# Performance work log

Measured on AMD Instinct MI355X. Metric: run time of the kernel, lower is better.

Reference implementation:

```python
import jax, jax.numpy as jnp
import numpy as np

N_NODES = 50000
N_EDGES = 800000
N_REL = 3
N_GRAPHS = 500
EMB = 128
IN_DIM = EMB * 3
HID = 256
N_CLASS = 10
N_SHAPE, N_COLOR, MAX_POS = 8, 8, 128


def rgcn_layer(h, src, dst, etype, W, root, b):
    """PyG RGCNConv with default aggr='mean':
    out[v] = sum_r mean_{(j->v) in E_r} h[j] @ W[r] + h[v] @ root + b
    Aggregate raw features per (dst, relation) bucket, then apply relation matmuls.
    """
    N, R = h.shape[0], W.shape[0]
    seg = dst * R + etype  # combined (node, relation) segment id
    sums = jax.ops.segment_sum(h[src], seg, num_segments=N * R)          # (N*R, d)
    cnt = jax.ops.segment_sum(jnp.ones(seg.shape, h.dtype), seg, num_segments=N * R)
    mean = (sums / jnp.maximum(cnt, 1.0)[:, None]).reshape(N, R, -1)     # (N, R, d)
    return jnp.einsum('nrd,rdh->nh', mean, W) + h @ root + b


def setup_inputs() -> dict:
    key = jax.random.key(0)
    ks = jax.random.split(key, 20)
    f32 = jnp.float32
    inp = {
        's': jax.random.randint(ks[0], (N_NODES,), 0, N_SHAPE),
        'c': jax.random.randint(ks[1], (N_NODES,), 0, N_COLOR),
        'p': jax.random.randint(ks[2], (N_NODES,), 0, MAX_POS),
        'edge_index': jax.random.randint(ks[3], (2, N_EDGES), 0, N_NODES),
        'edge_type': jax.random.randint(ks[4], (N_EDGES,), 0, N_REL),
        'batch': jnp.sort(jax.random.randint(ks[5], (N_NODES,), 0, N_GRAPHS)),
        'shape_emb': jax.random.normal(ks[6], (N_SHAPE, EMB), f32),
        'color_emb': jax.random.normal(ks[7], (N_COLOR, EMB), f32),
        'pos_emb': jax.random.normal(ks[8], (MAX_POS, EMB), f32),
        'W1': jax.random.normal(ks[9], (N_REL, IN_DIM, HID), f32) / np.sqrt(IN_DIM),
        'root1': jax.random.normal(ks[10], (IN_DIM, HID), f32) / np.sqrt(IN_DIM),
        'b1': jnp.zeros((HID,), f32),
        'W2': jax.random.normal(ks[11], (N_REL, HID, HID), f32) / np.sqrt(HID),
        'root2': jax.random.normal(ks[12], (HID, HID), f32) / np.sqrt(HID),
        'b2': jnp.zeros((HID,), f32),
        'lin_w': jax.random.normal(ks[13], (HID, N_CLASS), f32) / np.sqrt(HID),
        'lin_b': jnp.zeros((N_CLASS,), f32),
    }
    return inp


def reference(s, c, p, edge_index, edge_type, batch,
              shape_emb, color_emb, pos_emb,
              W1, root1, b1, W2, root2, b2, lin_w, lin_b):
    src, dst = edge_index[0], edge_index[1]
    h = jnp.concatenate([shape_emb[s], color_emb[c], pos_emb[p]], axis=-1)  # (N, 3*emb)
    h = jax.nn.relu(rgcn_layer(h, src, dst, edge_type, W1, root1, b1))
    h = jax.nn.relu(rgcn_layer(h, src, dst, edge_type, W2, root2, b2))
    # global_mean_pool over graphs
    gsum = jax.ops.segment_sum(h, batch, num_segments=N_GRAPHS)
    gcnt = jax.ops.segment_sum(jnp.ones((h.shape[0],), h.dtype), batch, num_segments=N_GRAPHS)
    pooled = gsum / jnp.maximum(gcnt, 1.0)[:, None]
    return pooled @ lin_w + lin_b
```

## Files before the change

kernel.cpp:

```cpp
#include <hip/hip_runtime.h>
#include <hip/hip_bf16.h>

#define NN 50000
#define NE 800000
#define NR 3
#define NG 500
#define NB (NN * NR)
#define NCLS 10
#define NCMB 8192
#define CHUNK 2048
#define NBLK ((NB + CHUNK - 1) / CHUNK)

#define P1_COMBO   196
#define P1_ZCNT    586
#define P1_ZPOOL   502
#define P1_TAB     576
#define P1_WF      1024
#define P1_TOTAL   (P1_COMBO + P1_ZCNT + P1_ZPOOL + P1_TAB + P1_WF)
#define P2_CNT     3125
#define P2_COMB    (4 * NCMB)
#define P2_TOTAL   (P2_CNT + P2_COMB)

typedef __hip_bfloat16 bf16;
typedef __attribute__((ext_vector_type(8))) short short8;
typedef __attribute__((ext_vector_type(4))) float floatx4;

static __device__ __forceinline__ float b2f(bf16 x) { return __bfloat162float(x); }
static __device__ __forceinline__ bf16  f2b(float x) { return __float2bfloat16(x); }
static __device__ __forceinline__ float bs2f(short x) {
    return __bfloat162float(*reinterpret_cast<const bf16*>(&x));
}
static __device__ __forceinline__ short f2bs(float x) {
    bf16 b = __float2bfloat16(x);
    return *reinterpret_cast<const short*>(&b);
}

__global__ __launch_bounds__(256) void prep1(const int* __restrict__ s,
                                             const int* __restrict__ c,
                                             const int* __restrict__ p,
                                             const float* __restrict__ se,
                                             const float* __restrict__ ce,
                                             const float* __restrict__ pe,
                                             const float* __restrict__ W1,
                                             const float* __restrict__ root1,
                                             const float* __restrict__ W2,
                                             const float* __restrict__ root2,
                                             int* __restrict__ combo,
                                             unsigned* __restrict__ cnt,
                                             unsigned* __restrict__ poolz,
                                             float* __restrict__ tab,
                                             bf16* __restrict__ Wf) {
    int b = blockIdx.x, t = threadIdx.x;
    if (b < P1_COMBO) {
        int n = b * 256 + t;
        if (n < NN) combo[n] = (s[n] << 10) | (c[n] << 7) | p[n];
        return;
    }
    b -= P1_COMBO;
    if (b < P1_ZCNT) {
        int i = b * 256 + t;
        if (i < NB) cnt[i] = 0u;
        return;
    }
    b -= P1_ZCNT;
    if (b < P1_ZPOOL) {
        int i = b * 256 + t;
        if (i < NG * 256 + NG) poolz[i] = 0u;
        return;
    }
    b -= P1_ZPOOL;
    if (b < P1_TAB) {
        int r = b / 144, row = b % 144;
        const float* A; int segk;
        if (row < 8)       { A = se + row * 128;        segk = 0; }
        else if (row < 16) { A = ce + (row - 8) * 128;  segk = 128; }
        else               { A = pe + (row - 16) * 128; segk = 256; }
        const float* W = (r < 3) ? (W1 + (size_t)r * 384 * 256) : root1;
        float acc = 0.f;
        for (int k = 0; k < 128; ++k)
            acc += A[k] * W[(size_t)(segk + k) * 256 + t];
        tab[((size_t)r * 144 + row) * 256 + t] = acc;
        return;
    }
    b -= P1_TAB;
    {
        int idx = b * 256 + t;
        int j     = idx & 7;
        int lane  = (idx >> 3) & 63;
        int ni    = (idx >> 9) & 3;
        int chunk = (idx >> 11) & 31;
        int colblk = idx >> 16;
        int col = colblk * 64 + ni * 16 + (lane & 15);
        int k   = chunk * 32 + (lane >> 4) * 8 + j;
        float v = (k < 768) ? W2[((size_t)(k >> 8) * 256 + (k & 255)) * 256 + col]
                            : root2[(size_t)(k - 768) * 256 + col];
        Wf[idx] = f2b(v);
    }
}

__global__ __launch_bounds__(256) void prep2(const int* __restrict__ ei,
                                             const int* __restrict__ et,
                                             int* __restrict__ cnt,
                                             const float* __restrict__ tab,
                                             const float* __restrict__ b1,
                                             bf16* __restrict__ comb) {
    int b = blockIdx.x, t = threadIdx.x;
    if (b < P2_CNT) {
        int e = b * 256 + t;
        if (e < NE) atomicAdd(&cnt[ei[NE + e] * NR + et[e]], 1);
        return;
    }
    b -= P2_CNT;
    {
        int r = b >> 13, cmb = b & (NCMB - 1);
        int si = cmb >> 10, ci = (cmb >> 7) & 7, pi = cmb & 127;
        const float* tr = tab + (size_t)r * 144 * 256;
        float v = tr[si * 256 + t] + tr[(8 + ci) * 256 + t] + tr[(16 + pi) * 256 + t];
        if (r == 3) v += b1[t];
        comb[(size_t)b * 256 + t] = f2b(v);
    }
}

__global__ __launch_bounds__(256) void scan_block_sums(const int* __restrict__ cnt,
                                                       int* __restrict__ bsum) {
    __shared__ int sm[256];
    int b = blockIdx.x, t = threadIdx.x;
    int base = b * CHUNK + t * 8, s = 0;
#pragma unroll
    for (int j = 0; j < 8; ++j) { int i = base + j; if (i < NB) s += cnt[i]; }
    sm[t] = s; __syncthreads();
    for (int st = 128; st; st >>= 1) { if (t < st) sm[t] += sm[t + st]; __syncthreads(); }
    if (!t) bsum[b] = sm[0];
}

__global__ __launch_bounds__(256) void scan_write(const int* __restrict__ cnt,
                                                  const int* __restrict__ bsum,
                                                  int* __restrict__ off,
                                                  int* __restrict__ cursor) {
    int b = blockIdx.x, t = threadIdx.x;
    int bbase = 0;
    for (int i = 0; i < b; ++i) bbase += bsum[i];
    if (b == 0 && t == 0) {
        int tot = 0;
        for (int i = 0; i < NBLK; ++i) tot += bsum[i];
        off[NB] = tot;
    }
    int base = b * CHUNK + t * 8;
    int v[8], ts = 0;
#pragma unroll
    for (int j = 0; j < 8; ++j) { int i = base + j; v[j] = (i < NB) ? cnt[i] : 0; ts += v[j]; }
    int lane = t & 63, wv = t >> 6;
    int incl = ts;
    for (int d = 1; d < 64; d <<= 1) {
        int o = __shfl_up(incl, d, 64);
        if (lane >= d) incl += o;
    }
    __shared__ int wsum[4];
    if (lane == 63) wsum[wv] = incl;
    __syncthreads();
    int wbase = 0;
    for (int w = 0; w < wv; ++w) wbase += wsum[w];
    int run = bbase + wbase + incl - ts;
#pragma unroll
    for (int j = 0; j < 8; ++j) {
        int i = base + j;
        if (i < NB) { off[i] = run; cursor[i] = run; }
        run += v[j];
    }
}

__global__ __launch_bounds__(256) void scatter_edges(const int* __restrict__ ei,
                                                     const int* __restrict__ et,
                                                     const int* __restrict__ combo,
                                                     int* __restrict__ cursor,
                                                     int2* __restrict__ esc) {
    int e = blockIdx.x * 256 + threadIdx.x;
    if (e >= NE) return;
    int b = ei[NE + e] * NR + et[e];
    int pos = atomicAdd(&cursor[b], 1);
    int s = ei[e];
    esc[pos] = make_int2(s, combo[s]);
}

__global__ __launch_bounds__(256) void l1_fused(const int* __restrict__ off,
                                                const int2* __restrict__ esc,
                                                const int* __restrict__ combo,
                                                const bf16* __restrict__ comb,
                                                bf16* __restrict__ h1) {
    int wave = threadIdx.x >> 6, lane = threadIdx.x & 63;
    int dst = blockIdx.x * 4 + wave;
    if (dst >= NN) return;
    int half = lane >> 5, li8 = (lane & 31) * 8;
    int o0 = off[dst * NR],     o1 = off[dst * NR + 1],
        o2 = off[dst * NR + 2], o3 = off[dst * NR + 3];
    short8 rootv = {};
    if (half == 0)
        rootv = *(const short8*)(comb + ((size_t)(3 * NCMB) + combo[dst]) * 256 + li8);
    const bf16* c0 = comb;
    const bf16* c1 = comb + (size_t)NCMB * 256;
    const bf16* c2 = comb + (size_t)2 * NCMB * 256;
    float s0[8] = {}, s1[8] = {}, s2[8] = {};
    int n = max((o1 - o0 + 1) >> 1, max((o2 - o1 + 1) >> 1, (o3 - o2 + 1) >> 1));
    for (int k = 0; k < n; k += 2) {
#pragma unroll
        for (int kk = 0; kk < 2; ++kk) {
            int i0 = o0 + 2 * (k + kk) + half;
            int i1 = o1 + 2 * (k + kk) + half;
            int i2 = o2 + 2 * (k + kk) + half;
            bool g0 = i0 < o1, g1 = i1 < o2, g2 = i2 < o3;
            int2 e0 = esc[g0 ? i0 : 0];
            int2 e1 = esc[g1 ? i1 : 0];
            int2 e2 = esc[g2 ? i2 : 0];
            short8 v0 = *(const short8*)(c0 + (size_t)(g0 ? e0.y : 0) * 256 + li8);
            short8 v1 = *(const short8*)(c1 + (size_t)(g1 ? e1.y : 0) * 256 + li8);
            short8 v2 = *(const short8*)(c2 + (size_t)(g2 ? e2.y : 0) * 256 + li8);
            float m0 = g0 ? 1.f : 0.f, m1 = g1 ? 1.f : 0.f, m2 = g2 ? 1.f : 0.f;
#pragma unroll
            for (int i = 0; i < 8; ++i) {
                s0[i] += bs2f(v0[i]) * m0;
                s1[i] += bs2f(v1[i]) * m1;
                s2[i] += bs2f(v2[i]) * m2;
            }
        }
    }
    float inv0 = (o1 > o0) ? 1.f / (float)(o1 - o0) : 0.f;
    float inv1 = (o2 > o1) ? 1.f / (float)(o2 - o1) : 0.f;
    float inv2 = (o3 > o2) ? 1.f / (float)(o3 - o2) : 0.f;
    short8 o;
#pragma unroll
    for (int i = 0; i < 8; ++i) {
        float t0 = s0[i] + __shfl_xor(s0[i], 32);
        float t1 = s1[i] + __shfl_xor(s1[i], 32);
        float t2 = s2[i] + __shfl_xor(s2[i], 32);
        float a = bs2f(rootv[i]) + t0 * inv0 + t1 * inv1 + t2 * inv2;
        o[i] = f2bs(fmaxf(a, 0.f));
    }
    if (half == 0)
        *(short8*)(h1 + (size_t)dst * 256 + li8) = o;
}

__global__ __launch_bounds__(256) void agg_all(const int* __restrict__ off,
                                               const int2* __restrict__ esc,
                                               const bf16* __restrict__ h1,
                                               bf16* __restrict__ hagg) {
    int wave = threadIdx.x >> 6, lane = threadIdx.x & 63;
    int dst = blockIdx.x * 4 + wave;
    if (dst >= NN) return;
    int half = lane >> 5, li8 = (lane & 31) * 8;
    int o0 = off[dst * NR],     o1 = off[dst * NR + 1],
        o2 = off[dst * NR + 2], o3 = off[dst * NR + 3];
    float s0[8] = {}, s1[8] = {}, s2[8] = {};
    int n = max((o1 - o0 + 1) >> 1, max((o2 - o1 + 1) >> 1, (o3 - o2 + 1) >> 1));
    for (int k = 0; k < n; k += 2) {
#pragma unroll
        for (int kk = 0; kk < 2; ++kk) {
            int i0 = o0 + 2 * (k + kk) + half;
            int i1 = o1 + 2 * (k + kk) + half;
            int i2 = o2 + 2 * (k + kk) + half;
            bool g0 = i0 < o1, g1 = i1 < o2, g2 = i2 < o3;
            int2 e0 = esc[g0 ? i0 : 0];
            int2 e1 = esc[g1 ? i1 : 0];
            int2 e2 = esc[g2 ? i2 : 0];
            short8 v0 = *(const short8*)(h1 + (size_t)(g0 ? e0.x : 0) * 256 + li8);
            short8 v1 = *(const short8*)(h1 + (size_t)(g1 ? e1.x : 0) * 256 + li8);
            short8 v2 = *(const short8*)(h1 + (size_t)(g2 ? e2.x : 0) * 256 + li8);
            float m0 = g0 ? 1.f : 0.f, m1 = g1 ? 1.f : 0.f, m2 = g2 ? 1.f : 0.f;
#pragma unroll
            for (int i = 0; i < 8; ++i) {
                s0[i] += bs2f(v0[i]) * m0;
                s1[i] += bs2f(v1[i]) * m1;
                s2[i] += bs2f(v2[i]) * m2;
            }
        }
    }
    float inv0 = (o1 > o0) ? 1.f / (float)(o1 - o0) : 0.f;
    float inv1 = (o2 > o1) ? 1.f / (float)(o2 - o1) : 0.f;
    float inv2 = (o3 > o2) ? 1.f / (float)(o3 - o2) : 0.f;
    short8 w0, w1, w2;
#pragma unroll
    for (int i = 0; i < 8; ++i) {
        float t0 = s0[i] + __shfl_xor(s0[i], 32);
        float t1 = s1[i] + __shfl_xor(s1[i], 32);
        float t2 = s2[i] + __shfl_xor(s2[i], 32);
        w0[i] = f2bs(t0 * inv0);
        w1[i] = f2bs(t1 * inv1);
        w2[i] = f2bs(t2 * inv2);
    }
    if (half == 0) {
        bf16* hd = hagg + (size_t)dst * 768 + li8;
        *(short8*)(hd)       = w0;
        *(short8*)(hd + 256) = w1;
        *(short8*)(hd + 512) = w2;
    }
}

__global__ __launch_bounds__(256) void gemm_cat(const bf16* __restrict__ hagg,
                                                const bf16* __restrict__ h1,
                                                const bf16* __restrict__ Wf,
                                                const float* __restrict__ bias,
                                                const int* __restrict__ batch,
                                                float* __restrict__ pool,
                                                float* __restrict__ gcnt) {
    __shared__ short lds[4][2][32 * 40];
    const int t = threadIdx.x;
    const int wave = t >> 6, lane = t & 63;
    const int quad = lane >> 4, l16 = lane & 15;
    const int row0 = blockIdx.x * 32;
    const int colblk = wave;
    const int rsub = lane >> 2;
    const int ksub = (lane & 3) * 8;
    short* A0 = lds[wave][0];
    short* A1 = lds[wave][1];

    const int r0 = min(row0 + rsub, NN - 1);
    const int r1 = min(row0 + 16 + rsub, NN - 1);
    const bf16* gA0 = hagg + (size_t)r0 * 768 + ksub;
    const bf16* gA1 = hagg + (size_t)r1 * 768 + ksub;
    const bf16* gH0 = h1 + (size_t)r0 * 256 + ksub;
    const bf16* gH1 = h1 + (size_t)r1 * 256 + ksub;
    const short8* bbase = (const short8*)Wf + (size_t)colblk * 32 * 4 * 64 + lane;

    auto loadA2 = [&](int k0, short8& a0, short8& a1) {
        if (k0 < 768) { a0 = *(const short8*)(gA0 + k0); a1 = *(const short8*)(gA1 + k0); }
        else          { a0 = *(const short8*)(gH0 + k0 - 768); a1 = *(const short8*)(gH1 + k0 - 768); }
    };
    auto loadB = [&](int chunk, short8* bf4) {
        const short8* bp = bbase + (size_t)chunk * 4 * 64;
#pragma unroll
        for (int ni = 0; ni < 4; ++ni) bf4[ni] = bp[ni * 64];
    };

    floatx4 acc[2][4] = {};
    short8 aE0, aE1, bE[4];
    short8 aO0, aO1, bO[4];
    loadA2(0, aE0, aE1);  loadB(0, bE);
    loadA2(32, aO0, aO1); loadB(1, bO);

#pragma unroll
    for (int i = 0; i < 32; i += 2) {
        *(short8*)&A0[rsub * 40 + ksub] = aE0;
        *(short8*)&A0[(16 + rsub) * 40 + ksub] = aE1;
        {
            short8 af0 = *(const short8*)&A0[l16 * 40 + quad * 8];
            short8 af1 = *(const short8*)&A0[(16 + l16) * 40 + quad * 8];
#pragma unroll
            for (int ni = 0; ni < 4; ++ni) {
                acc[0][ni] = __builtin_amdgcn_mfma_f32_16x16x32_bf16(af0, bE[ni], acc[0][ni], 0, 0, 0);
                acc[1][ni] = __builtin_amdgcn_mfma_f32_16x16x32_bf16(af1, bE[ni], acc[1][ni], 0, 0, 0);
            }
        }
        if (i + 2 < 32) { loadA2((i + 2) * 32, aE0, aE1); loadB(i + 2, bE); }
        *(short8*)&A1[rsub * 40 + ksub] = aO0;
        *(short8*)&A1[(16 + rsub) * 40 + ksub] = aO1;
        {
            short8 af0 = *(const short8*)&A1[l16 * 40 + quad * 8];
            short8 af1 = *(const short8*)&A1[(16 + l16) * 40 + quad * 8];
#pragma unroll
            for (int ni = 0; ni < 4; ++ni) {
                acc[0][ni] = __builtin_amdgcn_mfma_f32_16x16x32_bf16(af0, bO[ni], acc[0][ni], 0, 0, 0);
                acc[1][ni] = __builtin_amdgcn_mfma_f32_16x16x32_bf16(af1, bO[ni], acc[1][ni], 0, 0, 0);
            }
        }
        if (i + 3 < 32) { loadA2((i + 3) * 32, aO0, aO1); loadB(i + 3, bO); }
    }

    __syncthreads();
    short* st = &lds[0][0][0];
#pragma unroll
    for (int mi = 0; mi < 2; ++mi) {
#pragma unroll
        for (int ni = 0; ni < 4; ++ni) {
            int n = colblk * 64 + ni * 16 + l16;
            float bn = bias[n];
#pragma unroll
            for (int ii = 0; ii < 4; ++ii) {
                int lrow = mi * 16 + quad * 4 + ii;
                float v = (row0 + lrow < NN) ? fmaxf(acc[mi][ni][ii] + bn, 0.f) : 0.f;
                st[lrow * 260 + n] = f2bs(v);
            }
        }
    }
    __syncthreads();
    int nrows = NN - row0; if (nrows > 32) nrows = 32;
    int curg = batch[row0];
    float a = 0.f, cntf = 0.f;
    for (int rr = 0; rr < nrows; ++rr) {
        int g = batch[row0 + rr];
        if (g != curg) {
            atomicAdd(&pool[(size_t)curg * 256 + t], a);
            if (t == 0) atomicAdd(&gcnt[curg], cntf);
            a = 0.f; cntf = 0.f; curg = g;
        }
        a += bs2f(st[rr * 260 + t]);
        cntf += 1.f;
    }
    atomicAdd(&pool[(size_t)curg * 256 + t], a);
    if (t == 0) atomicAdd(&gcnt[curg], cntf);
}

__global__ __launch_bounds__(256) void final_head(const float* __restrict__ pool,
                                                  const float* __restrict__ gcnt,
                                                  const float* __restrict__ lin_w,
                                                  const float* __restrict__ lin_b,
                                                  float* __restrict__ out) {
    __shared__ float sm[256];
    int g = blockIdx.x, t = threadIdx.x;
    float inv = 1.0f / fmaxf(gcnt[g], 1.0f);
    sm[t] = pool[(size_t)g * 256 + t] * inv;
    __syncthreads();
    if (t < NCLS) {
        float s = lin_b[t];
        for (int d = 0; d < 256; ++d) s += sm[d] * lin_w[d * NCLS + t];
        out[g * NCLS + t] = s;
    }
}

extern "C" void kernel_launch(void* const* d_in, const int* in_sizes, int n_in,
                              void* d_out, int out_size, void* d_ws, size_t ws_size,
                              hipStream_t stream) {
    const int*   s_idx = (const int*)d_in[0];
    const int*   c_idx = (const int*)d_in[1];
    const int*   p_idx = (const int*)d_in[2];
    const int*   ei    = (const int*)d_in[3];
    const int*   et    = (const int*)d_in[4];
    const int*   batch = (const int*)d_in[5];
    const float* se    = (const float*)d_in[6];
    const float* ce    = (const float*)d_in[7];
    const float* pe    = (const float*)d_in[8];
    const float* W1    = (const float*)d_in[9];
    const float* root1 = (const float*)d_in[10];
    const float* b1    = (const float*)d_in[11];
    const float* W2    = (const float*)d_in[12];
    const float* root2 = (const float*)d_in[13];
    const float* b2    = (const float*)d_in[14];
    const float* lin_w = (const float*)d_in[15];
    const float* lin_b = (const float*)d_in[16];
    float* out = (float*)d_out;

    char* w = (char*)d_ws;
    size_t o = 0;
    auto alloc = [&](size_t bytes) -> void* {
        o = (o + 15) & ~(size_t)15;
        void* ptr = w + o;
        o += bytes;
        return ptr;
    };
    bf16*  hagg   = (bf16*) alloc((size_t)NN * 768 * 2);
    bf16*  h1     = (bf16*) alloc((size_t)NN * 256 * 2);
    bf16*  comb   = (bf16*) alloc((size_t)4 * NCMB * 256 * 2);
    int*   combo  = (int*)  alloc((size_t)NN * 4);
    int2*  esc    = (int2*) alloc((size_t)NE * 8);
    int*   cnt    = (int*)  alloc((size_t)NB * 4);
    int*   off    = (int*)  alloc((size_t)(NB + 1) * 4);
    int*   cursor = (int*)  alloc((size_t)NB * 4);
    int*   bsum   = (int*)  alloc((size_t)NBLK * 4);
    float* tab    = (float*)alloc((size_t)4 * 144 * 256 * 4);
    bf16*  Wf     = (bf16*) alloc((size_t)256 * 1024 * 2);
    float* pool   = (float*)alloc((size_t)NG * 256 * 4);
    float* gcnt  = (float*)alloc((size_t)NG * 4);
    (void)ws_size;

    prep1<<<P1_TOTAL, 256, 0, stream>>>(s_idx, c_idx, p_idx, se, ce, pe,
                                        W1, root1, W2, root2,
                                        combo, (unsigned*)cnt, (unsigned*)pool, tab, Wf);
    prep2<<<P2_TOTAL, 256, 0, stream>>>(ei, et, cnt, tab, b1, comb);
    scan_block_sums<<<NBLK, 256, 0, stream>>>(cnt, bsum);
    scan_write<<<NBLK, 256, 0, stream>>>(cnt, bsum, off, cursor);
    scatter_edges<<<(NE + 255) / 256, 256, 0, stream>>>(ei, et, combo, cursor, esc);
    l1_fused<<<(NN + 3) / 4, 256, 0, stream>>>(off, esc, combo, comb, h1);
    agg_all<<<(NN + 3) / 4, 256, 0, stream>>>(off, esc, h1, hagg);
    gemm_cat<<<(NN + 31) / 32, 256, 0, stream>>>(hagg, h1, Wf, b2, batch, pool, gcnt);
    final_head<<<NG, 256, 0, stream>>>(pool, gcnt, lin_w, lin_b, out);
}
```

Before: 383.3 us.

## Pack edge records into 32-bit words and flatten layer-1 gather loop

Edge records shrink from an int2 (source, combo) to one 32-bit word holding the source shifted by 13 bits with the 13-bit combo in the low bits. This halves the edge-array footprint written by the scatter and read by both aggregation kernels. Layer-1 aggregation now walks the node's contiguous edge range for all three relations together, unrolled four ways. Each edge picks its relation table and 1/count weight from its position against the bucket offsets, so lanes no longer idle while they wait for the longest relation. The packing assumes node ids fit in 19 bits and combo ids in 13, which holds for these sizes.

```diff
diff --git a/kernel.cpp b/kernel.cpp
--- a/kernel.cpp
+++ b/kernel.cpp
@@ -173,17 +173,17 @@
                                                      const int* __restrict__ et,
                                                      const int* __restrict__ combo,
                                                      int* __restrict__ cursor,
-                                                     int2* __restrict__ esc) {
+                                                     unsigned* __restrict__ esc) {
     int e = blockIdx.x * 256 + threadIdx.x;
     if (e >= NE) return;
     int b = ei[NE + e] * NR + et[e];
     int pos = atomicAdd(&cursor[b], 1);
     int s = ei[e];
-    esc[pos] = make_int2(s, combo[s]);
+    esc[pos] = ((unsigned)s << 13) | (unsigned)combo[s];
 }
 
 __global__ __launch_bounds__(256) void l1_fused(const int* __restrict__ off,
-                                                const int2* __restrict__ esc,
+                                                const unsigned* __restrict__ esc,
                                                 const int* __restrict__ combo,
                                                 const bf16* __restrict__ comb,
                                                 bf16* __restrict__ h1) {
@@ -191,56 +191,66 @@
     int dst = blockIdx.x * 4 + wave;
     if (dst >= NN) return;
     int half = lane >> 5, li8 = (lane & 31) * 8;
-    int o0 = off[dst * NR],     o1 = off[dst * NR + 1],
-        o2 = off[dst * NR + 2], o3 = off[dst * NR + 3];
+    int b0 = dst * NR;
+    int o0 = off[b0], o1 = off[b0 + 1], o2 = off[b0 + 2], o3 = off[b0 + 3];
+    float inv0 = (o1 > o0) ? 1.f / (float)(o1 - o0) : 0.f;
+    float inv1 = (o2 > o1) ? 1.f / (float)(o2 - o1) : 0.f;
+    float inv2 = (o3 > o2) ? 1.f / (float)(o3 - o2) : 0.f;
     short8 rootv = {};
     if (half == 0)
         rootv = *(const short8*)(comb + ((size_t)(3 * NCMB) + combo[dst]) * 256 + li8);
-    const bf16* c0 = comb;
-    const bf16* c1 = comb + (size_t)NCMB * 256;
-    const bf16* c2 = comb + (size_t)2 * NCMB * 256;
-    float s0[8] = {}, s1[8] = {}, s2[8] = {};
-    int n = max((o1 - o0 + 1) >> 1, max((o2 - o1 + 1) >> 1, (o3 - o2 + 1) >> 1));
-    for (int k = 0; k < n; k += 2) {
-#pragma unroll
-        for (int kk = 0; kk < 2; ++kk) {
-            int i0 = o0 + 2 * (k + kk) + half;
-            int i1 = o1 + 2 * (k + kk) + half;
-            int i2 = o2 + 2 * (k + kk) + half;
-            bool g0 = i0 < o1, g1 = i1 < o2, g2 = i2 < o3;
-            int2 e0 = esc[g0 ? i0 : 0];
-            int2 e1 = esc[g1 ? i1 : 0];
-            int2 e2 = esc[g2 ? i2 : 0];
-            short8 v0 = *(const short8*)(c0 + (size_t)(g0 ? e0.y : 0) * 256 + li8);
-            short8 v1 = *(const short8*)(c1 + (size_t)(g1 ? e1.y : 0) * 256 + li8);
-            short8 v2 = *(const short8*)(c2 + (size_t)(g2 ? e2.y : 0) * 256 + li8);
-            float m0 = g0 ? 1.f : 0.f, m1 = g1 ? 1.f : 0.f, m2 = g2 ? 1.f : 0.f;
-#pragma unroll
-            for (int i = 0; i < 8; ++i) {
-                s0[i] += bs2f(v0[i]) * m0;
-                s1[i] += bs2f(v1[i]) * m1;
-                s2[i] += bs2f(v2[i]) * m2;
-            }
-        }
-    }
-    float inv0 = (o1 > o0) ? 1.f / (float)(o1 - o0) : 0.f;
-    float inv1 = (o2 > o1) ? 1.f / (float)(o2 - o1) : 0.f;
-    float inv2 = (o3 > o2) ? 1.f / (float)(o3 - o2) : 0.f;
+    float s[8] = {};
+    int j = o0;
+    for (; j + 8 <= o3; j += 8) {
+        int k0 = j + half, k1 = j + 2 + half, k2 = j + 4 + half, k3 = j + 6 + half;
+        unsigned e0 = esc[k0], e1 = esc[k1], e2 = esc[k2], e3 = esc[k3];
+        int ro0 = ((k0 >= o1) ? NCMB : 0) + ((k0 >= o2) ? NCMB : 0);
+        int ro1 = ((k1 >= o1) ? NCMB : 0) + ((k1 >= o2) ? NCMB : 0);
+        int ro2 = ((k2 >= o1) ? NCMB : 0) + ((k2 >= o2) ? NCMB : 0);
+        int ro3 = ((k3 >= o1) ? NCMB : 0) + ((k3 >= o2) ? NCMB : 0);
+        short8 v0 = *(const short8*)(comb + (size_t)(ro0 + (e0 & (NCMB - 1))) * 256 + li8);
+        short8 v1 = *(const short8*)(comb + (size_t)(ro1 + (e1 & (NCMB - 1))) * 256 + li8);
+        short8 v2 = *(const short8*)(comb + (size_t)(ro2 + (e2 & (NCMB - 1))) * 256 + li8);
+        short8 v3 = *(const short8*)(comb + (size_t)(ro3 + (e3 & (NCMB - 1))) * 256 + li8);
+        float w0 = (k0 >= o2) ? inv2 : ((k0 >= o1) ? inv1 : inv0);
+        float w1 = (k1 >= o2) ? inv2 : ((k1 >= o1) ? inv1 : inv0);
+        float w2 = (k2 >= o2) ? inv2 : ((k2 >= o1) ? inv1 : inv0);
+        float w3 = (k3 >= o2) ? inv2 : ((k3 >= o1) ? inv1 : inv0);
+#pragma unroll
+        for (int i = 0; i < 8; ++i)
+            s[i] += bs2f(v0[i]) * w0 + bs2f(v1[i]) * w1
+                  + bs2f(v2[i]) * w2 + bs2f(v3[i]) * w3;
+    }
+    for (; j + 2 <= o3; j += 2) {
+        int k0 = j + half;
+        unsigned e0 = esc[k0];
+        int ro0 = ((k0 >= o1) ? NCMB : 0) + ((k0 >= o2) ? NCMB : 0);
+        short8 v0 = *(const short8*)(comb + (size_t)(ro0 + (e0 & (NCMB - 1))) * 256 + li8);
+        float w0 = (k0 >= o2) ? inv2 : ((k0 >= o1) ? inv1 : inv0);
+#pragma unroll
+        for (int i = 0; i < 8; ++i) s[i] += bs2f(v0[i]) * w0;
+    }
+    if (j < o3 && half == 0) {
+        int k0 = j;
+        unsigned e0 = esc[k0];
+        int ro0 = ((k0 >= o1) ? NCMB : 0) + ((k0 >= o2) ? NCMB : 0);
+        short8 v0 = *(const short8*)(comb + (size_t)(ro0 + (e0 & (NCMB - 1))) * 256 + li8);
+        float w0 = (k0 >= o2) ? inv2 : ((k0 >= o1) ? inv1 : inv0);
+#pragma unroll
+        for (int i = 0; i < 8; ++i) s[i] += bs2f(v0[i]) * w0;
+    }
     short8 o;
 #pragma unroll
     for (int i = 0; i < 8; ++i) {
-        float t0 = s0[i] + __shfl_xor(s0[i], 32);
-        float t1 = s1[i] + __shfl_xor(s1[i], 32);
-        float t2 = s2[i] + __shfl_xor(s2[i], 32);
-        float a = bs2f(rootv[i]) + t0 * inv0 + t1 * inv1 + t2 * inv2;
-        o[i] = f2bs(fmaxf(a, 0.f));
+        float tot = s[i] + __shfl_xor(s[i], 32);
+        o[i] = f2bs(fmaxf(bs2f(rootv[i]) + tot, 0.f));
     }
     if (half == 0)
         *(short8*)(h1 + (size_t)dst * 256 + li8) = o;
 }
 
 __global__ __launch_bounds__(256) void agg_all(const int* __restrict__ off,
-                                               const int2* __restrict__ esc,
+                                               const unsigned* __restrict__ esc,
                                                const bf16* __restrict__ h1,
                                                bf16* __restrict__ hagg) {
     int wave = threadIdx.x >> 6, lane = threadIdx.x & 63;
@@ -258,12 +268,12 @@
             int i1 = o1 + 2 * (k + kk) + half;
             int i2 = o2 + 2 * (k + kk) + half;
             bool g0 = i0 < o1, g1 = i1 < o2, g2 = i2 < o3;
-            int2 e0 = esc[g0 ? i0 : 0];
-            int2 e1 = esc[g1 ? i1 : 0];
-            int2 e2 = esc[g2 ? i2 : 0];
-            short8 v0 = *(const short8*)(h1 + (size_t)(g0 ? e0.x : 0) * 256 + li8);
-            short8 v1 = *(const short8*)(h1 + (size_t)(g1 ? e1.x : 0) * 256 + li8);
-            short8 v2 = *(const short8*)(h1 + (size_t)(g2 ? e2.x : 0) * 256 + li8);
+            unsigned e0 = esc[g0 ? i0 : 0];
+            unsigned e1 = esc[g1 ? i1 : 0];
+            unsigned e2 = esc[g2 ? i2 : 0];
+            short8 v0 = *(const short8*)(h1 + (size_t)(g0 ? (e0 >> 13) : 0) * 256 + li8);
+            short8 v1 = *(const short8*)(h1 + (size_t)(g1 ? (e1 >> 13) : 0) * 256 + li8);
+            short8 v2 = *(const short8*)(h1 + (size_t)(g2 ? (e2 >> 13) : 0) * 256 + li8);
             float m0 = g0 ? 1.f : 0.f, m1 = g1 ? 1.f : 0.f, m2 = g2 ? 1.f : 0.f;
 #pragma unroll
             for (int i = 0; i < 8; ++i) {
@@ -445,19 +455,19 @@
         o += bytes;
         return ptr;
     };
-    bf16*  hagg   = (bf16*) alloc((size_t)NN * 768 * 2);
-    bf16*  h1     = (bf16*) alloc((size_t)NN * 256 * 2);
-    bf16*  comb   = (bf16*) alloc((size_t)4 * NCMB * 256 * 2);
-    int*   combo  = (int*)  alloc((size_t)NN * 4);
-    int2*  esc    = (int2*) alloc((size_t)NE * 8);
-    int*   cnt    = (int*)  alloc((size_t)NB * 4);
-    int*   off    = (int*)  alloc((size_t)(NB + 1) * 4);
-    int*   cursor = (int*)  alloc((size_t)NB * 4);
-    int*   bsum   = (int*)  alloc((size_t)NBLK * 4);
-    float* tab    = (float*)alloc((size_t)4 * 144 * 256 * 4);
-    bf16*  Wf     = (bf16*) alloc((size_t)256 * 1024 * 2);
-    float* pool   = (float*)alloc((size_t)NG * 256 * 4);
-    float* gcnt  = (float*)alloc((size_t)NG * 4);
+    bf16*     hagg   = (bf16*)    alloc((size_t)NN * 768 * 2);
+    bf16*     h1     = (bf16*)    alloc((size_t)NN * 256 * 2);
+    bf16*     comb   = (bf16*)    alloc((size_t)4 * NCMB * 256 * 2);
+    int*      combo  = (int*)     alloc((size_t)NN * 4);
+    unsigned* esc    = (unsigned*)alloc((size_t)NE * 4);
+    int*      cnt    = (int*)     alloc((size_t)NB * 4);
+    int*      off    = (int*)     alloc((size_t)(NB + 1) * 4);
+    int*      cursor = (int*)     alloc((size_t)NB * 4);
+    int*      bsum   = (int*)     alloc((size_t)NBLK * 4);
+    float*    tab    = (float*)   alloc((size_t)4 * 144 * 256 * 4);
+    bf16*     Wf     = (bf16*)    alloc((size_t)256 * 1024 * 2);
+    float*    pool   = (float*)   alloc((size_t)NG * 256 * 4);
+    float*    gcnt   = (float*)   alloc((size_t)NG * 4);
     (void)ws_size;
 
     prep1<<<P1_TOTAL, 256, 0, stream>>>(s_idx, c_idx, p_idx, se, ce, pe,
```

New measurement: 375.7 us. 1.02x faster.
